# Kernel tuning notes

Hardware: AMD Instinct MI355X
Metric: run time of the kernel (lower is better)

The kernel has to match this reference:

```python
import jax, jax.numpy as jnp
import numpy as np

DIM = 768
HEADS = 12
HEAD_DIM = DIM // HEADS  # 64, must equal 2*ROPE_DIM
HIDDEN = int(DIM * 4 * 2 / 3)  # 2048
EPS = 1e-6


def _ln(x, w, b, eps=EPS):
    mu = jnp.mean(x, -1, keepdims=True)
    var = jnp.mean((x - mu) ** 2, -1, keepdims=True)
    return (x - mu) * jax.lax.rsqrt(var + eps) * w + b


def _rotate_half(x):
    xr = x.reshape(x.shape[:-1] + (-1, 2))
    return jnp.stack((-xr[..., 1], xr[..., 0]), -1).reshape(x.shape)


def _rope_tables(H, W):
    # Matches get_rope: dim=32 per axis, pt_seq_len=16, theta=10000
    dim, pt, theta = 32, 16.0, 10000.0
    freqs = 1.0 / theta ** (np.arange(0, dim, 2, dtype=np.float32) / dim)  # [16]
    fH = np.repeat((np.arange(H, dtype=np.float32) / H * pt)[:, None] * freqs[None, :], 2, axis=-1)  # [H,32]
    fW = np.repeat((np.arange(W, dtype=np.float32) / W * pt)[:, None] * freqs[None, :], 2, axis=-1)  # [W,32]
    f = np.concatenate([np.broadcast_to(fH[:, None, :], (H, W, dim)),
                        np.broadcast_to(fW[None, :, :], (H, W, dim))], -1)  # [H,W,64]
    f = f.reshape(H * W, 2 * dim)
    return jnp.asarray(np.cos(f)), jnp.asarray(np.sin(f))


def block_forward(x, ln1_w, ln1_b, q_w, q_b, k_w, v_w, v_b, proj_w, proj_b,
                  ln2_w, ln2_b, w1_w, w1_b, w2_w, w2_b, ffn_w, ffn_b, w3_w, w3_b, ws):
    B, H, W, C = x.shape
    shortcut = x
    h = _ln(x, ln1_w, ln1_b)
    # window partition with padding
    pad_h = (-H) % ws
    pad_w = (-W) % ws
    h = jnp.pad(h, ((0, 0), (0, pad_h), (0, pad_w), (0, 0)))
    Hp, Wp = H + pad_h, W + pad_w
    h = h.reshape(B, Hp // ws, ws, Wp // ws, ws, C).transpose(0, 1, 3, 2, 4, 5).reshape(-1, ws, ws, C)
    Bw = h.shape[0]
    N = ws * ws
    t = h.reshape(Bw, N, C)
    q = t @ q_w + q_b  # k has no bias
    k = t @ k_w
    v = t @ v_w + v_b
    q = q.reshape(Bw, N, HEADS, HEAD_DIM).transpose(0, 2, 1, 3)  # [Bw,h,N,d]
    k = k.reshape(Bw, N, HEADS, HEAD_DIM).transpose(0, 2, 1, 3)
    v = v.reshape(Bw, N, HEADS, HEAD_DIM).transpose(0, 2, 1, 3)
    cos, sin = _rope_tables(ws, ws)  # [N, 64]
    q = q * cos + _rotate_half(q) * sin
    k = k * cos + _rotate_half(k) * sin
    scale = HEAD_DIM ** (-0.5)
    attn = jax.nn.softmax(jnp.einsum('bhnd,bhmd->bhnm', q * scale, k), axis=-1)
    o = jnp.einsum('bhnm,bhmd->bhnd', attn, v).transpose(0, 2, 1, 3).reshape(Bw, N, -1)
    o = o @ proj_w + proj_b
    o = o.reshape(Bw, ws, ws, C)
    # window unpartition
    o = o.reshape(B, Hp // ws, Wp // ws, ws, ws, C).transpose(0, 1, 3, 2, 4, 5).reshape(B, Hp, Wp, C)
    o = o[:, :H, :W, :]
    x = shortcut + o
    # SwiGLU MLP with sub-LN
    h = _ln(x, ln2_w, ln2_b)
    hid = jax.nn.silu(h @ w1_w + w1_b) * (h @ w2_w + w2_b)
    hid = _ln(hid, ffn_w, ffn_b)
    return x + hid @ w3_w + w3_b


def setup_inputs() -> dict:
    key = jax.random.key(0)
    ks = jax.random.split(key, 9)
    s = 0.02
    d = {
        'x': jax.random.normal(ks[0], (8, 64, 64, DIM), jnp.float32),
        'ln1_w': jnp.ones((DIM,), jnp.float32),
        'ln1_b': jnp.zeros((DIM,), jnp.float32),
        'q_w': jax.random.normal(ks[1], (DIM, DIM), jnp.float32) * s,
        'q_b': jnp.zeros((DIM,), jnp.float32),
        'k_w': jax.random.normal(ks[2], (DIM, DIM), jnp.float32) * s,
        'v_w': jax.random.normal(ks[3], (DIM, DIM), jnp.float32) * s,
        'v_b': jnp.zeros((DIM,), jnp.float32),
        'proj_w': jax.random.normal(ks[4], (DIM, DIM), jnp.float32) * s,
        'proj_b': jnp.zeros((DIM,), jnp.float32),
        'ln2_w': jnp.ones((DIM,), jnp.float32),
        'ln2_b': jnp.zeros((DIM,), jnp.float32),
        'w1_w': jax.random.normal(ks[5], (DIM, HIDDEN), jnp.float32) * s,
        'w1_b': jnp.zeros((HIDDEN,), jnp.float32),
        'w2_w': jax.random.normal(ks[6], (DIM, HIDDEN), jnp.float32) * s,
        'w2_b': jnp.zeros((HIDDEN,), jnp.float32),
        'ffn_w': jnp.ones((HIDDEN,), jnp.float32),
        'ffn_b': jnp.zeros((HIDDEN,), jnp.float32),
        'w3_w': jax.random.normal(ks[7], (HIDDEN, DIM), jnp.float32) * s,
        'w3_b': jnp.zeros((DIM,), jnp.float32),
        'window_size': 14,
    }
    return d


def reference(x, ln1_w, ln1_b, q_w, q_b, k_w, v_w, v_b, proj_w, proj_b,
              ln2_w, ln2_b, w1_w, w1_b, w2_w, w2_b, ffn_w, ffn_b, w3_w, w3_b, window_size):
    return block_forward(x, ln1_w, ln1_b, q_w, q_b, k_w, v_w, v_b, proj_w, proj_b,
                         ln2_w, ln2_b, w1_w, w1_b, w2_w, w2_b, ffn_w, ffn_b, w3_w, w3_b,
                         int(window_size))
```

## Files before the change

kernel.cpp:

```cpp
#include <hip/hip_runtime.h>
#include <hip/hip_bf16.h>
#include <stdint.h>

typedef unsigned short u16;
typedef unsigned int u32;
typedef __attribute__((ext_vector_type(4))) float f32x4;
typedef __attribute__((ext_vector_type(8))) short s16x8;
typedef __attribute__((ext_vector_type(4))) u32 u32x4;

#define DEV __device__ __forceinline__
#define AS1 __attribute__((address_space(1)))
#define AS3 __attribute__((address_space(3)))

constexpr int T2 = 8 * 64 * 64;
constexpr int C = 768;
constexpr int HID = 2048;
constexpr int CHUNK = 8192;
constexpr int QKVS = 2304;

DEV float blo(u32 u) { return __uint_as_float(u << 16); }
DEV float bhi(u32 u) { return __uint_as_float(u & 0xffff0000u); }
DEV float b2f(u16 u) { return __uint_as_float((u32)u << 16); }
DEV u16 f2bf(float f) {
  u32 x = __float_as_uint(f);
  u32 r = x + 0x7fffu + ((x >> 16) & 1u);
  return (u16)(r >> 16);
}
DEV u32 pack2(float a, float b) { return (u32)f2bf(a) | ((u32)f2bf(b) << 16); }
DEV u32 cvtpk(float lo, float hi) {
  u32 r;
  asm("v_cvt_pk_bf16_f32 %0, %1, %2" : "=v"(r) : "v"(lo), "v"(hi));
  return r;
}

template <int NW>
DEV void reduce2(float& s, float& q) {
#pragma unroll
  for (int o = 32; o > 0; o >>= 1) {
    s += __shfl_down(s, o);
    q += __shfl_down(q, o);
  }
  __shared__ float ps[2 * NW];
  int wave = threadIdx.x >> 6, lane = threadIdx.x & 63;
  if (lane == 0) { ps[wave] = s; ps[NW + wave] = q; }
  __syncthreads();
  s = 0.f; q = 0.f;
#pragma unroll
  for (int i = 0; i < NW; ++i) { s += ps[i]; q += ps[NW + i]; }
}

__global__ __launch_bounds__(256) void transpose_cvt_tiled_k(
    const float* __restrict__ src, u16* __restrict__ dst, int K, int N, int rs, int ro) {
  __shared__ float t[32][33];
  int k0 = blockIdx.x * 32, n0 = blockIdx.y * 32;
  int tx = threadIdx.x, ty = threadIdx.y;
#pragma unroll
  for (int j = 0; j < 4; ++j)
    t[ty + j * 8][tx] = src[(size_t)(k0 + ty + j * 8) * N + n0 + tx];
  __syncthreads();
#pragma unroll
  for (int j = 0; j < 4; ++j) {
    int n = n0 + ty + j * 8;
    dst[((size_t)n * rs + ro) * K + k0 + tx] = f2bf(t[tx][ty + j * 8]);
  }
}

__global__ void build_biases_k(const float* __restrict__ qb, const float* __restrict__ vbb,
                               const float* __restrict__ w1b, const float* __restrict__ w2b,
                               float* __restrict__ qkvb, float* __restrict__ w12b) {
  int i = blockIdx.x * 256 + threadIdx.x;
  if (i < 2304)
    qkvb[i] = i < 768 ? qb[i] : (i < 1536 ? 0.f : vbb[i - 1536]);
  int j = i - 2304;
  if (j >= 0 && j < 4096) w12b[j] = (j & 1) ? w2b[j >> 1] : w1b[j >> 1];
}

__global__ void rope_tables_k(float* __restrict__ ct, float* __restrict__ st) {
  int i = blockIdx.x * 256 + threadIdx.x;
  if (i >= 196 * 32) return;
  int n = i >> 5, jp = i & 31;
  int d = jp << 1;
  int r = n / 14, c = n - r * 14;
  float pos, fj;
  if (d < 32) { pos = (float)r * (16.f / 14.f); fj = (float)(d >> 1); }
  else        { pos = (float)c * (16.f / 14.f); fj = (float)((d - 32) >> 1); }
  float fr = __expf(fj * (-2.f / 32.f) * logf(10000.f));
  float ang = pos * fr;
  float cv = cosf(ang), sv = sinf(ang);
  ct[n * 64 + d] = cv; ct[n * 64 + d + 1] = cv;
  st[n * 64 + d] = sv; st[n * 64 + d + 1] = sv;
}

__global__ __launch_bounds__(256) void ln_k(const float* __restrict__ in,
    const float* __restrict__ w, const float* __restrict__ bb, u16* __restrict__ out) {
  size_t row = blockIdx.x;
  int tid = threadIdx.x;
  const float* xr = in + row * C;
  float v0 = xr[tid], v1 = xr[tid + 256], v2 = xr[tid + 512];
  float s = v0 + v1 + v2, q = v0 * v0 + v1 * v1 + v2 * v2;
  reduce2<4>(s, q);
  float mu = s * (1.f / 768.f), var = q * (1.f / 768.f) - mu * mu;
  float rs = rsqrtf(var + 1e-6f);
  u16* orow = out + row * C;
  orow[tid]       = f2bf((v0 - mu) * rs * w[tid]       + bb[tid]);
  orow[tid + 256] = f2bf((v1 - mu) * rs * w[tid + 256] + bb[tid + 256]);
  orow[tid + 512] = f2bf((v2 - mu) * rs * w[tid + 512] + bb[tid + 512]);
}

__global__ __launch_bounds__(384) void ln_bf16_k(const u16* __restrict__ in,
    const float* __restrict__ w, const float* __restrict__ bb, u16* __restrict__ out) {
  size_t row = blockIdx.x;
  int t = threadIdx.x;
  u32 u = ((const u32*)(in + row * C))[t];
  float v0 = blo(u), v1 = bhi(u);
  float s = v0 + v1, q = v0 * v0 + v1 * v1;
  reduce2<6>(s, q);
  float mu = s * (1.f / 768.f), var = q * (1.f / 768.f) - mu * mu;
  float rs = rsqrtf(var + 1e-6f);
  float o0 = (v0 - mu) * rs * w[2 * t] + bb[2 * t];
  float o1 = (v1 - mu) * rs * w[2 * t + 1] + bb[2 * t + 1];
  ((u32*)(out + row * C))[t] = cvtpk(o0, o1);
}

DEV float rope1(float v, float p, int r, int d, bool odd, bool isq,
                const float* __restrict__ ct, const float* __restrict__ st) {
  int rem = r & 4095;
  int n = ((rem >> 6) % 14) * 14 + ((rem & 63) % 14);
  float c = ct[n * 64 + d], s = st[n * 64 + d];
  float o = odd ? (v * c + p * s) : (v * c - p * s);
  return isq ? o * 0.125f : o;
}

template <int EPI>
__global__ __launch_bounds__(256) void gemm_k(
    const u16* __restrict__ A, const u16* __restrict__ Bt,
    const float* __restrict__ bias, void* __restrict__ Cout,
    const void* __restrict__ resid, int M, int Nn, int K, int lda,
    const float* __restrict__ ct, const float* __restrict__ st) {
  __shared__ u16 LDS[128 * 128];
  u16* As = LDS;
  u16* Bs = LDS + 8192;
  const int tid = threadIdx.x;
  const int wave = tid >> 6, lane = tid & 63;
  const int wm = wave >> 1, wn = wave & 1;
  const int gx = gridDim.x;
  const int id = blockIdx.y * gx + blockIdx.x;
  const int xcd = id & 7;
  const int j0 = id >> 3;
  const int W = gx >> 3;
  const int per_sub = gridDim.y << 3;
  const int sub = j0 / per_sub;
  const int jj = j0 - sub * per_sub;
  const int tm = xcd * W + (sub << 3) + (jj & 7);
  const int tn = jj >> 3;
  const int l16 = lane & 15, lq = lane >> 4;

  f32x4 acc[4][4];
#pragma unroll
  for (int a = 0; a < 4; ++a)
#pragma unroll
    for (int b = 0; b < 4; ++b)
#pragma unroll
      for (int e = 0; e < 4; ++e) acc[a][b][e] = 0.f;

  const int nk = K >> 6;
  for (int kt = 0; kt < nk; ++kt) {
    const int k0 = kt << 6;
#pragma unroll
    for (int i = 0; i < 4; ++i) {
      int row = (((wave << 2) + i) << 3) + (lane >> 3);
      int cl = (lane & 7) ^ (row & 7);
      const u16* sa = A + (size_t)(tm * 128 + row) * lda + k0 + cl * 8;
      __builtin_amdgcn_global_load_lds((const AS1 u32*)sa,
          (AS3 u32*)(As + (((wave << 2) + i) << 9)), 16, 0, 0);
      const u16* sb = Bt + (size_t)(tn * 128 + row) * K + k0 + cl * 8;
      __builtin_amdgcn_global_load_lds((const AS1 u32*)sb,
          (AS3 u32*)(Bs + (((wave << 2) + i) << 9)), 16, 0, 0);
    }
    asm volatile("s_waitcnt vmcnt(0)" ::: "memory");
    __syncthreads();
#pragma unroll
    for (int ks = 0; ks < 2; ++ks) {
      s16x8 af[4], bfr[4];
#pragma unroll
      for (int mf = 0; mf < 4; ++mf) {
        int row = (wm << 6) + (mf << 4) + l16;
        int sc = ((ks << 2) + lq) ^ (row & 7);
        af[mf] = *(const s16x8*)(As + row * 64 + sc * 8);
      }
#pragma unroll
      for (int nf = 0; nf < 4; ++nf) {
        int row = (wn << 6) + (nf << 4) + l16;
        int sc = ((ks << 2) + lq) ^ (row & 7);
        bfr[nf] = *(const s16x8*)(Bs + row * 64 + sc * 8);
      }
      __builtin_amdgcn_s_setprio(1);
#pragma unroll
      for (int mf = 0; mf < 4; ++mf)
#pragma unroll
        for (int nf = 0; nf < 4; ++nf)
          acc[mf][nf] =
              __builtin_amdgcn_mfma_f32_16x16x32_bf16(af[mf], bfr[nf], acc[mf][nf], 0, 0, 0);
      __builtin_amdgcn_s_setprio(0);
    }
    __syncthreads();
  }

  if constexpr (EPI == 2) {
#pragma unroll
    for (int nf = 0; nf < 4; ++nf) {
      int col = (tn << 7) + (wn << 6) + (nf << 4) + l16;
      float bs = bias[col];
      const u16* rp = (const u16*)resid;
#pragma unroll
      for (int mf = 0; mf < 4; ++mf) {
        int rbase = (tm << 7) + (wm << 6) + (mf << 4) + (lq << 2);
#pragma unroll
        for (int j = 0; j < 4; ++j) {
          size_t idx = (size_t)(rbase + j) * Nn + col;
          ((float*)Cout)[idx] = b2f(rp[idx]) + acc[mf][nf][j] + bs;
        }
      }
    }
  } else {
#pragma unroll
    for (int nf = 0; nf < 4; ++nf) {
      int lcol = (wn << 6) + (nf << 4) + l16;
      int col = (tn << 7) + lcol;
      float bs = bias[col];
#pragma unroll
      for (int mf = 0; mf < 4; ++mf) {
        int rloc = (wm << 6) + (mf << 4) + (lq << 2);
        float v[4];
#pragma unroll
        for (int j = 0; j < 4; ++j) v[j] = acc[mf][nf][j] + bs;
        if constexpr (EPI == 1) {
          const float* rp = (const float*)resid;
#pragma unroll
          for (int j = 0; j < 4; ++j)
            v[j] += rp[(size_t)(tm * 128 + rloc + j) * Nn + col];
        }
        if constexpr (EPI == 3) {
          float pv[4];
#pragma unroll
          for (int j = 0; j < 4; ++j) pv[j] = __shfl_xor(v[j], 1);
          if (col < 1536) {
            bool odd = (l16 & 1) != 0, isq = col < 768;
            int d = col & 63;
#pragma unroll
            for (int j = 0; j < 4; ++j)
              v[j] = rope1(v[j], pv[j], tm * 128 + rloc + j, d, odd, isq, ct, st);
          }
        }
#pragma unroll
        for (int j = 0; j < 4; ++j) {
          int row = rloc + j;
          int byte = row * 256 + ((lcol * 2) ^ ((row & 7) << 4));
          *(u16*)((char*)LDS + byte) = f2bf(v[j]);
        }
      }
    }
    __syncthreads();
    u16* Cb = (u16*)Cout + (size_t)(tm * 128) * Nn + (tn << 7);
    int chunk = tid & 15;
#pragma unroll
    for (int it = 0; it < 8; ++it) {
      int row = (tid >> 4) + it * 16;
      int byte = row * 256 + ((chunk * 16) ^ ((row & 7) << 4));
      u32x4 val = *(const u32x4*)((const char*)LDS + byte);
      *(u32x4*)(Cb + (size_t)row * Nn + chunk * 8) = val;
    }
  }
}

__global__ __launch_bounds__(256) void attn_mfma_k(u16* __restrict__ qkv,
    const float* __restrict__ vb) {
  __shared__ u16 Vt[64 * 224];
  __shared__ u16 Pl[4 * 16 * 40];
  __shared__ int rowTab[208];
  int wid = blockIdx.x / 12, h = blockIdx.x - wid * 12;
  int bi = wid / 25, wr = wid - bi * 25;
  int hi = wr / 5, wj = wr - hi * 5;
  int rh = (hi == 4) ? 8 : 14, rw = (wj == 4) ? 8 : 14;
  int nv = rh * rw;
  int nk16 = (nv + 15) >> 4;
  int kvfull = nk16 >> 1;
  int nsteps = kvfull + (nk16 & 1);
  int vcols = ((nk16 + 1) >> 1) << 5;
  int tid = threadIdx.x;
  int rowbase = (bi * 64 + hi * 14) * 64 + wj * 14;

  if (tid < 208) {
    int mk = tid < nv ? tid : nv - 1;
    int nr = mk / rw, nc = mk - nr * rw;
    rowTab[tid] = rowbase + nr * 64 + nc;
  }
  __syncthreads();
  for (int idx = tid; idx < vcols * 32; idx += 256) {
    int key = idx >> 5, dp = idx & 31;
    int d = dp << 1;
    u32 val;
    if (key < nv) {
      size_t off = (size_t)rowTab[key] * QKVS + 1536 + (h << 6) + d;
      val = *(const u32*)(qkv + off);
    } else {
      val = pack2(vb[(h << 6) + d], vb[(h << 6) + d + 1]);
    }
    int b0 = (d * 448 + key * 2) ^ ((d & 7) << 4);
    int b1 = ((d + 1) * 448 + key * 2) ^ (((d + 1) & 7) << 4);
    Vt[b0 >> 1] = (u16)(val & 0xffffu);
    Vt[b1 >> 1] = (u16)(val >> 16);
  }
  __syncthreads();

  int wave = tid >> 6, lane = tid & 63;
  int l16 = lane & 15, lq = lane >> 4;
  u16* Pw = Pl + wave * 640;
  const u16* kbase = qkv + 768 + (h << 6);
  float vbr[4];
#pragma unroll
  for (int dt = 0; dt < 4; ++dt) vbr[dt] = vb[(h << 6) + dt * 16 + l16];

  int mtiles = (nv + 15) >> 4;
  for (int mt = wave; mt < mtiles; mt += 4) {
    s16x8 a[2];
    {
      int qi = mt * 16 + l16;
      const u16* qp = qkv + (size_t)rowTab[qi] * QKVS + (h << 6);
      a[0] = *(const s16x8*)(qp + lq * 8);
      a[1] = *(const s16x8*)(qp + 32 + lq * 8);
    }
    f32x4 O[4];
#pragma unroll
    for (int dt = 0; dt < 4; ++dt)
#pragma unroll
      for (int j = 0; j < 4; ++j) O[dt][j] = 0.f;
    float lrow[4] = {0.f, 0.f, 0.f, 0.f};

    for (int kv = 0; kv < nsteps; ++kv) {
      const bool full = kv < kvfull;
      const int keyb = kv << 5;
      f32x4 s0 = {0.f, 0.f, 0.f, 0.f}, s1 = {0.f, 0.f, 0.f, 0.f};
      int key0 = keyb + l16, key1 = key0 + 16;
      const u16* kr0 = kbase + (size_t)rowTab[key0] * QKVS;
      const u16* kr1 = full ? (kbase + (size_t)rowTab[key1] * QKVS) : kbase;
      __builtin_amdgcn_s_setprio(1);
#pragma unroll
      for (int s = 0; s < 2; ++s) {
        s16x8 b0 = *(const s16x8*)(kr0 + s * 32 + lq * 8);
        s0 = __builtin_amdgcn_mfma_f32_16x16x32_bf16(a[s], b0, s0, 0, 0, 0);
        if (full) {
          s16x8 b1 = *(const s16x8*)(kr1 + s * 32 + lq * 8);
          s1 = __builtin_amdgcn_mfma_f32_16x16x32_bf16(a[s], b1, s1, 0, 0, 0);
        }
      }
      __builtin_amdgcn_s_setprio(0);
#pragma unroll
      for (int j = 0; j < 4; ++j) {
        float p0 = key0 < nv ? __expf(s0[j]) : (key0 < 196 ? 1.f : 0.f);
        float p1 = full ? (key1 < nv ? __expf(s1[j]) : (key1 < 196 ? 1.f : 0.f)) : 0.f;
        float rs = p0 + p1;
        rs += __shfl_xor(rs, 1);
        rs += __shfl_xor(rs, 2);
        rs += __shfl_xor(rs, 4);
        rs += __shfl_xor(rs, 8);
        lrow[j] += rs;
        u32 pk = cvtpk(p0, p1);
        Pw[(lq * 4 + j) * 40 + l16] = (u16)pk;
        Pw[(lq * 4 + j) * 40 + l16 + 16] = (u16)(pk >> 16);
      }
      s16x8 pa = *(const s16x8*)(Pw + l16 * 40 + lq * 8);
      __builtin_amdgcn_s_setprio(1);
#pragma unroll
      for (int dt = 0; dt < 4; ++dt) {
        int d = dt * 16 + l16;
        int vbyte = (d * 448 + keyb * 2 + lq * 16) ^ ((d & 7) << 4);
        s16x8 bv = *(const s16x8*)(Vt + (vbyte >> 1));
        O[dt] = __builtin_amdgcn_mfma_f32_16x16x32_bf16(pa, bv, O[dt], 0, 0, 0);
      }
      __builtin_amdgcn_s_setprio(0);
    }
    int Prem = 196 - (nk16 << 4);
    if (Prem > 0) {
#pragma unroll
      for (int j = 0; j < 4; ++j) {
        lrow[j] += (float)Prem;
#pragma unroll
        for (int dt = 0; dt < 4; ++dt) O[dt][j] += (float)Prem * vbr[dt];
      }
    }
#pragma unroll
    for (int j = 0; j < 4; ++j) {
      int qi = mt * 16 + lq * 4 + j;
      if (qi < nv) {
        float inv = 1.f / lrow[j];
        u16* op = qkv + (size_t)rowTab[qi] * QKVS + (h << 6);
#pragma unroll
        for (int dt = 0; dt < 4; ++dt) op[dt * 16 + l16] = f2bf(O[dt][j] * inv);
      }
    }
  }
}

__global__ __launch_bounds__(256) void swiglu_ln_k(u16* __restrict__ h12,
    const float* __restrict__ w, const float* __restrict__ bb) {
  size_t row = blockIdx.x;
  int tid = threadIdx.x;
  const u32x4 ua = *(const u32x4*)(h12 + row * 4096 + tid * 16);
  const u32x4 ub = *(const u32x4*)(h12 + row * 4096 + tid * 16 + 8);
  u32 pp[8] = {ua.x, ua.y, ua.z, ua.w, ub.x, ub.y, ub.z, ub.w};
  float g[8];
  float s = 0.f, qq = 0.f;
#pragma unroll
  for (int j = 0; j < 8; ++j) {
    float a = blo(pp[j]), b = bhi(pp[j]);
    float sl = a / (1.f + __expf(-a));
    g[j] = sl * b;
    s += g[j];
    qq += g[j] * g[j];
  }
  reduce2<4>(s, qq);
  float mu = s * (1.f / 2048.f);
  float var = qq * (1.f / 2048.f) - mu * mu;
  float rs = rsqrtf(var + 1e-6f);
  const float* wp = w + tid * 8;
  const float* bp = bb + tid * 8;
  u32 o4[4];
#pragma unroll
  for (int j = 0; j < 4; ++j) {
    float o0 = (g[2 * j] - mu) * rs * wp[2 * j] + bp[2 * j];
    float o1 = (g[2 * j + 1] - mu) * rs * wp[2 * j + 1] + bp[2 * j + 1];
    o4[j] = cvtpk(o0, o1);
  }
  *(u32x4*)(h12 + row * 4096 + tid * 8) = (u32x4){o4[0], o4[1], o4[2], o4[3]};
}

extern "C" void kernel_launch(void* const* d_in, const int* in_sizes, int n_in,
                              void* d_out, int out_size, void* d_ws, size_t ws_size,
                              hipStream_t stream) {
  const float* x    = (const float*)d_in[0];
  const float* ln1w = (const float*)d_in[1];
  const float* ln1b = (const float*)d_in[2];
  const float* qw   = (const float*)d_in[3];
  const float* qb   = (const float*)d_in[4];
  const float* kw   = (const float*)d_in[5];
  const float* vw   = (const float*)d_in[6];
  const float* vb   = (const float*)d_in[7];
  const float* pw   = (const float*)d_in[8];
  const float* pb   = (const float*)d_in[9];
  const float* ln2w = (const float*)d_in[10];
  const float* ln2b = (const float*)d_in[11];
  const float* w1   = (const float*)d_in[12];
  const float* w1b  = (const float*)d_in[13];
  const float* w2   = (const float*)d_in[14];
  const float* w2b  = (const float*)d_in[15];
  const float* ffw  = (const float*)d_in[16];
  const float* ffb  = (const float*)d_in[17];
  const float* w3   = (const float*)d_in[18];
  const float* w3b  = (const float*)d_in[19];

  char* ws = (char*)d_ws;
  size_t off = 0;
  auto alloc = [&](size_t bytes) -> char* {
    char* p = ws + off;
    off += (bytes + 255) & ~(size_t)255;
    return p;
  };
  u16* qkvwt = (u16*)alloc((size_t)QKVS * 768 * 2);
  u16* pwt   = (u16*)alloc((size_t)768 * 768 * 2);
  u16* w12t  = (u16*)alloc((size_t)4096 * 768 * 2);
  u16* w3t   = (u16*)alloc((size_t)768 * 2048 * 2);
  float* qkvb = (float*)alloc((size_t)QKVS * 4);
  float* w12b = (float*)alloc((size_t)4096 * 4);
  float* ct = (float*)alloc((size_t)196 * 64 * 4);
  float* st = (float*)alloc((size_t)196 * 64 * 4);
  u16* xw  = (u16*)alloc((size_t)T2 * C * 2);
  u16* qkv = (u16*)alloc((size_t)T2 * QKVS * 2);
  u16* x2b  = xw;
  u16* h2   = qkv;
  u16* h12c = qkv + (size_t)T2 * C;
  float* outp = (float*)d_out;

  dim3 tb(32, 8);
  transpose_cvt_tiled_k<<<dim3(24, 24), tb, 0, stream>>>(qw, qkvwt, 768, 768, 1, 0);
  transpose_cvt_tiled_k<<<dim3(24, 24), tb, 0, stream>>>(kw, qkvwt + (size_t)768 * 768, 768, 768, 1, 0);
  transpose_cvt_tiled_k<<<dim3(24, 24), tb, 0, stream>>>(vw, qkvwt + (size_t)1536 * 768, 768, 768, 1, 0);
  transpose_cvt_tiled_k<<<dim3(24, 24), tb, 0, stream>>>(pw, pwt, 768, 768, 1, 0);
  transpose_cvt_tiled_k<<<dim3(24, 64), tb, 0, stream>>>(w1, w12t, 768, 2048, 2, 0);
  transpose_cvt_tiled_k<<<dim3(24, 64), tb, 0, stream>>>(w2, w12t, 768, 2048, 2, 1);
  transpose_cvt_tiled_k<<<dim3(64, 24), tb, 0, stream>>>(w3, w3t, 2048, 768, 1, 0);
  build_biases_k<<<25, 256, 0, stream>>>(qb, vb, w1b, w2b, qkvb, w12b);
  rope_tables_k<<<(196 * 32 + 255) / 256, 256, 0, stream>>>(ct, st);

  ln_k<<<T2, 256, 0, stream>>>(x, ln1w, ln1b, xw);
  gemm_k<3><<<dim3(T2 / 128, QKVS / 128), 256, 0, stream>>>(
      xw, qkvwt, qkvb, qkv, nullptr, T2, QKVS, 768, 768, ct, st);
  attn_mfma_k<<<200 * 12, 256, 0, stream>>>(qkv, vb);
  gemm_k<1><<<dim3(T2 / 128, 6), 256, 0, stream>>>(
      qkv, pwt, pb, x2b, x, T2, 768, 768, QKVS, nullptr, nullptr);

  ln_bf16_k<<<T2, 384, 0, stream>>>(x2b, ln2w, ln2b, h2);
  for (int cidx = 0; cidx < T2 / CHUNK; ++cidx) {
    const u16* hrow = h2 + (size_t)cidx * CHUNK * C;
    gemm_k<0><<<dim3(CHUNK / 128, 32), 256, 0, stream>>>(
        hrow, w12t, w12b, h12c, nullptr, CHUNK, 4096, 768, 768, nullptr, nullptr);
    swiglu_ln_k<<<CHUNK, 256, 0, stream>>>(h12c, ffw, ffb);
    gemm_k<2><<<dim3(CHUNK / 128, 6), 256, 0, stream>>>(
        h12c, w3t, w3b, outp + (size_t)cidx * CHUNK * C,
        x2b + (size_t)cidx * CHUNK * C, CHUNK, 768, 2048, 4096, nullptr, nullptr);
  }
}
```

Baseline: 1.059 ms.

## Add 256x256 double-buffered GEMM with async LDS loads and fused RoPE epilogue

Adds a new 512-thread GEMM kernel with 256x256 output tiles, double-buffered LDS staging through global_load_lds, and a prefetch of the next K tile during compute. It is used for the QKV, projection and W1/W2 GEMMs. RoPE moves to the coalesced store phase using a packed cos/sin float2 table, replacing per-element table loads and shuffles. The W3 GEMM stays on the old 128-tile kernel, now specialised to its residual epilogue. The 128KB LDS footprint and larger accumulator arrays limit occupancy, and the bigger tiles mean fewer blocks for the smaller GEMMs.

```diff
diff --git a/kernel.cpp b/kernel.cpp
--- a/kernel.cpp
+++ b/kernel.cpp
@@ -75,20 +75,17 @@
   if (j >= 0 && j < 4096) w12b[j] = (j & 1) ? w2b[j >> 1] : w1b[j >> 1];
 }
 
-__global__ void rope_tables_k(float* __restrict__ ct, float* __restrict__ st) {
+__global__ void rope_tables_k(float2* __restrict__ csp) {
   int i = blockIdx.x * 256 + threadIdx.x;
   if (i >= 196 * 32) return;
-  int n = i >> 5, jp = i & 31;
-  int d = jp << 1;
+  int n = i >> 5, dp = i & 31;
   int r = n / 14, c = n - r * 14;
   float pos, fj;
-  if (d < 32) { pos = (float)r * (16.f / 14.f); fj = (float)(d >> 1); }
-  else        { pos = (float)c * (16.f / 14.f); fj = (float)((d - 32) >> 1); }
+  if (dp < 16) { pos = (float)r * (16.f / 14.f); fj = (float)dp; }
+  else         { pos = (float)c * (16.f / 14.f); fj = (float)(dp - 16); }
   float fr = __expf(fj * (-2.f / 32.f) * logf(10000.f));
   float ang = pos * fr;
-  float cv = cosf(ang), sv = sinf(ang);
-  ct[n * 64 + d] = cv; ct[n * 64 + d + 1] = cv;
-  st[n * 64 + d] = sv; st[n * 64 + d + 1] = sv;
+  csp[i] = make_float2(cosf(ang), sinf(ang));
 }
 
 __global__ __launch_bounds__(256) void ln_k(const float* __restrict__ in,
@@ -122,24 +119,155 @@
   ((u32*)(out + row * C))[t] = cvtpk(o0, o1);
 }
 
-DEV float rope1(float v, float p, int r, int d, bool odd, bool isq,
-                const float* __restrict__ ct, const float* __restrict__ st) {
-  int rem = r & 4095;
-  int n = ((rem >> 6) % 14) * 14 + ((rem & 63) % 14);
-  float c = ct[n * 64 + d], s = st[n * 64 + d];
-  float o = odd ? (v * c + p * s) : (v * c - p * s);
-  return isq ? o * 0.125f : o;
-}
-
 template <int EPI>
-__global__ __launch_bounds__(256) void gemm_k(
+__global__ __launch_bounds__(512, 2) void gemm256_k(
     const u16* __restrict__ A, const u16* __restrict__ Bt,
     const float* __restrict__ bias, void* __restrict__ Cout,
     const void* __restrict__ resid, int M, int Nn, int K, int lda,
-    const float* __restrict__ ct, const float* __restrict__ st) {
-  __shared__ u16 LDS[128 * 128];
-  u16* As = LDS;
-  u16* Bs = LDS + 8192;
+    const float2* __restrict__ csp) {
+  __shared__ u16 LDS[65536];
+  const int tid = threadIdx.x;
+  const int wave = tid >> 6, lane = tid & 63;
+  const int wm = wave >> 2, wn = wave & 3;
+  const int l16 = lane & 15, lq = lane >> 4;
+  const int gx = gridDim.x;
+  const int id = blockIdx.y * gx + blockIdx.x;
+  const int xcd = id & 7;
+  const int j0 = id >> 3;
+  const int W = gx >> 3;
+  const int SW = W < 8 ? W : 8;
+  const int per_sub = gridDim.y * SW;
+  const int sub = j0 / per_sub;
+  const int jj = j0 - sub * per_sub;
+  const int tm = xcd * W + sub * SW + (jj & (SW - 1));
+  const int tn = jj / SW;
+
+  f32x4 acc[8][4];
+#pragma unroll
+  for (int a = 0; a < 8; ++a)
+#pragma unroll
+    for (int b = 0; b < 4; ++b)
+#pragma unroll
+      for (int e = 0; e < 4; ++e) acc[a][b][e] = 0.f;
+
+  const int nk = K >> 6;
+  auto STAGE = [&](int kt, int buf) {
+    const int k0 = kt << 6;
+    u16* Ad = LDS + buf * 32768;
+    u16* Bd = Ad + 16384;
+#pragma unroll
+    for (int i = 0; i < 4; ++i) {
+      int blk = (wave << 2) + i;
+      int row = (blk << 3) + (lane >> 3);
+      int cl = (lane & 7) ^ (row & 7);
+      const u16* sa = A + (size_t)(tm * 256 + row) * lda + k0 + cl * 8;
+      __builtin_amdgcn_global_load_lds((const AS1 u32*)sa, (AS3 u32*)(Ad + (blk << 9)),
+                                       16, 0, 0);
+      const u16* sb = Bt + (size_t)(tn * 256 + row) * K + k0 + cl * 8;
+      __builtin_amdgcn_global_load_lds((const AS1 u32*)sb, (AS3 u32*)(Bd + (blk << 9)),
+                                       16, 0, 0);
+    }
+  };
+
+  STAGE(0, 0);
+  asm volatile("s_waitcnt vmcnt(0)" ::: "memory");
+  __syncthreads();
+  for (int t = 0; t < nk; ++t) {
+    const int cur = t & 1;
+    if (t + 1 < nk) STAGE(t + 1, cur ^ 1);
+    const u16* As = LDS + cur * 32768;
+    const u16* Bs = As + 16384;
+#pragma unroll
+    for (int ks = 0; ks < 2; ++ks) {
+      s16x8 bfr[4];
+#pragma unroll
+      for (int nf = 0; nf < 4; ++nf) {
+        int row = (wn << 6) + (nf << 4) + l16;
+        int sc = ((ks << 2) + lq) ^ (row & 7);
+        bfr[nf] = *(const s16x8*)(Bs + row * 64 + sc * 8);
+      }
+      __builtin_amdgcn_s_setprio(1);
+#pragma unroll
+      for (int mf = 0; mf < 8; ++mf) {
+        int row = (wm << 7) + (mf << 4) + l16;
+        int sc = ((ks << 2) + lq) ^ (row & 7);
+        s16x8 af = *(const s16x8*)(As + row * 64 + sc * 8);
+#pragma unroll
+        for (int nf = 0; nf < 4; ++nf)
+          acc[mf][nf] =
+              __builtin_amdgcn_mfma_f32_16x16x32_bf16(af, bfr[nf], acc[mf][nf], 0, 0, 0);
+      }
+      __builtin_amdgcn_s_setprio(0);
+    }
+    asm volatile("s_waitcnt vmcnt(0)" ::: "memory");
+    __syncthreads();
+  }
+
+#pragma unroll
+  for (int nf = 0; nf < 4; ++nf) {
+    int lcol = (wn << 6) + (nf << 4) + l16;
+    int col = (tn << 8) + lcol;
+    float bs = bias[col];
+#pragma unroll
+    for (int mf = 0; mf < 8; ++mf) {
+      int rloc = (wm << 7) + (mf << 4) + (lq << 2);
+      float v[4];
+#pragma unroll
+      for (int j = 0; j < 4; ++j) v[j] = acc[mf][nf][j] + bs;
+      if constexpr (EPI == 1) {
+        const float* rp = (const float*)resid;
+#pragma unroll
+        for (int j = 0; j < 4; ++j)
+          v[j] += rp[(size_t)(tm * 256 + rloc + j) * Nn + col];
+      }
+#pragma unroll
+      for (int j = 0; j < 4; ++j) {
+        int row = rloc + j;
+        int byte = row * 512 + ((lcol * 2) ^ ((row & 7) << 4));
+        *(u16*)((char*)LDS + byte) = f2bf(v[j]);
+      }
+    }
+  }
+  __syncthreads();
+  u16* Cb = (u16*)Cout + (size_t)(tm * 256) * Nn + (tn << 8);
+  const int chunk = tid & 31;
+  const int cbase = (tn << 8) + chunk * 8;
+  const bool inqk = cbase < 1536, isq = cbase < 768;
+  const int dp0 = (cbase & 63) >> 1;
+#pragma unroll
+  for (int it = 0; it < 16; ++it) {
+    int row = (tid >> 5) + it * 16;
+    int byte = row * 512 + ((chunk * 16) ^ ((row & 7) << 4));
+    u32x4 val = *(const u32x4*)((const char*)LDS + byte);
+    if constexpr (EPI == 3) {
+      if (inqk) {
+        int tok = tm * 256 + row;
+        int rem = tok & 4095;
+        int n = ((rem >> 6) % 14) * 14 + ((rem & 63) % 14);
+        const float2* cp = csp + n * 32 + dp0;
+        u32 wv[4] = {val.x, val.y, val.z, val.w};
+#pragma unroll
+        for (int p = 0; p < 4; ++p) {
+          float2 cs = cp[p];
+          float e = blo(wv[p]), o = bhi(wv[p]);
+          float re = e * cs.x - o * cs.y;
+          float ro = o * cs.x + e * cs.y;
+          if (isq) { re *= 0.125f; ro *= 0.125f; }
+          wv[p] = cvtpk(re, ro);
+        }
+        val = (u32x4){wv[0], wv[1], wv[2], wv[3]};
+      }
+    }
+    *(u32x4*)(Cb + (size_t)row * Nn + chunk * 8) = val;
+  }
+}
+
+__global__ __launch_bounds__(256) void gemm_k(
+    const u16* __restrict__ A, const u16* __restrict__ Bt,
+    const float* __restrict__ bias, float* __restrict__ Cout,
+    const u16* __restrict__ resid, int M, int Nn, int K, int lda) {
+  __shared__ u16 As[128 * 64];
+  __shared__ u16 Bs[128 * 64];
   const int tid = threadIdx.x;
   const int wave = tid >> 6, lane = tid & 63;
   const int wm = wave >> 1, wn = wave & 1;
@@ -148,11 +276,12 @@
   const int xcd = id & 7;
   const int j0 = id >> 3;
   const int W = gx >> 3;
-  const int per_sub = gridDim.y << 3;
+  const int SW = W < 8 ? W : 8;
+  const int per_sub = gridDim.y * SW;
   const int sub = j0 / per_sub;
   const int jj = j0 - sub * per_sub;
-  const int tm = xcd * W + (sub << 3) + (jj & 7);
-  const int tn = jj >> 3;
+  const int tm = xcd * W + sub * SW + (jj & (SW - 1));
+  const int tn = jj / SW;
   const int l16 = lane & 15, lq = lane >> 4;
 
   f32x4 acc[4][4];
@@ -205,70 +334,18 @@
     }
     __syncthreads();
   }
-
-  if constexpr (EPI == 2) {
-#pragma unroll
-    for (int nf = 0; nf < 4; ++nf) {
-      int col = (tn << 7) + (wn << 6) + (nf << 4) + l16;
-      float bs = bias[col];
-      const u16* rp = (const u16*)resid;
-#pragma unroll
-      for (int mf = 0; mf < 4; ++mf) {
-        int rbase = (tm << 7) + (wm << 6) + (mf << 4) + (lq << 2);
-#pragma unroll
-        for (int j = 0; j < 4; ++j) {
-          size_t idx = (size_t)(rbase + j) * Nn + col;
-          ((float*)Cout)[idx] = b2f(rp[idx]) + acc[mf][nf][j] + bs;
-        }
-      }
-    }
-  } else {
-#pragma unroll
-    for (int nf = 0; nf < 4; ++nf) {
-      int lcol = (wn << 6) + (nf << 4) + l16;
-      int col = (tn << 7) + lcol;
-      float bs = bias[col];
-#pragma unroll
-      for (int mf = 0; mf < 4; ++mf) {
-        int rloc = (wm << 6) + (mf << 4) + (lq << 2);
-        float v[4];
-#pragma unroll
-        for (int j = 0; j < 4; ++j) v[j] = acc[mf][nf][j] + bs;
-        if constexpr (EPI == 1) {
-          const float* rp = (const float*)resid;
-#pragma unroll
-          for (int j = 0; j < 4; ++j)
-            v[j] += rp[(size_t)(tm * 128 + rloc + j) * Nn + col];
-        }
-        if constexpr (EPI == 3) {
-          float pv[4];
-#pragma unroll
-          for (int j = 0; j < 4; ++j) pv[j] = __shfl_xor(v[j], 1);
-          if (col < 1536) {
-            bool odd = (l16 & 1) != 0, isq = col < 768;
-            int d = col & 63;
-#pragma unroll
-            for (int j = 0; j < 4; ++j)
-              v[j] = rope1(v[j], pv[j], tm * 128 + rloc + j, d, odd, isq, ct, st);
-          }
-        }
-#pragma unroll
-        for (int j = 0; j < 4; ++j) {
-          int row = rloc + j;
-          int byte = row * 256 + ((lcol * 2) ^ ((row & 7) << 4));
-          *(u16*)((char*)LDS + byte) = f2bf(v[j]);
-        }
-      }
-    }
-    __syncthreads();
-    u16* Cb = (u16*)Cout + (size_t)(tm * 128) * Nn + (tn << 7);
-    int chunk = tid & 15;
-#pragma unroll
-    for (int it = 0; it < 8; ++it) {
-      int row = (tid >> 4) + it * 16;
-      int byte = row * 256 + ((chunk * 16) ^ ((row & 7) << 4));
-      u32x4 val = *(const u32x4*)((const char*)LDS + byte);
-      *(u32x4*)(Cb + (size_t)row * Nn + chunk * 8) = val;
+#pragma unroll
+  for (int nf = 0; nf < 4; ++nf) {
+    int col = (tn << 7) + (wn << 6) + (nf << 4) + l16;
+    float bs = bias[col];
+#pragma unroll
+    for (int mf = 0; mf < 4; ++mf) {
+      int rbase = (tm << 7) + (wm << 6) + (mf << 4) + (lq << 2);
+#pragma unroll
+      for (int j = 0; j < 4; ++j) {
+        size_t idx = (size_t)(rbase + j) * Nn + col;
+        Cout[idx] = b2f(resid[idx]) + acc[mf][nf][j] + bs;
+      }
     }
   }
 }
@@ -472,8 +549,7 @@
   u16* w3t   = (u16*)alloc((size_t)768 * 2048 * 2);
   float* qkvb = (float*)alloc((size_t)QKVS * 4);
   float* w12b = (float*)alloc((size_t)4096 * 4);
-  float* ct = (float*)alloc((size_t)196 * 64 * 4);
-  float* st = (float*)alloc((size_t)196 * 64 * 4);
+  float2* csp = (float2*)alloc((size_t)196 * 32 * 8);
   u16* xw  = (u16*)alloc((size_t)T2 * C * 2);
   u16* qkv = (u16*)alloc((size_t)T2 * QKVS * 2);
   u16* x2b  = xw;
@@ -490,23 +566,23 @@
   transpose_cvt_tiled_k<<<dim3(24, 64), tb, 0, stream>>>(w2, w12t, 768, 2048, 2, 1);
   transpose_cvt_tiled_k<<<dim3(64, 24), tb, 0, stream>>>(w3, w3t, 2048, 768, 1, 0);
   build_biases_k<<<25, 256, 0, stream>>>(qb, vb, w1b, w2b, qkvb, w12b);
-  rope_tables_k<<<(196 * 32 + 255) / 256, 256, 0, stream>>>(ct, st);
+  rope_tables_k<<<25, 256, 0, stream>>>(csp);
 
   ln_k<<<T2, 256, 0, stream>>>(x, ln1w, ln1b, xw);
-  gemm_k<3><<<dim3(T2 / 128, QKVS / 128), 256, 0, stream>>>(
-      xw, qkvwt, qkvb, qkv, nullptr, T2, QKVS, 768, 768, ct, st);
+  gemm256_k<3><<<dim3(T2 / 256, QKVS / 256), 512, 0, stream>>>(
+      xw, qkvwt, qkvb, qkv, nullptr, T2, QKVS, 768, 768, csp);
   attn_mfma_k<<<200 * 12, 256, 0, stream>>>(qkv, vb);
-  gemm_k<1><<<dim3(T2 / 128, 6), 256, 0, stream>>>(
-      qkv, pwt, pb, x2b, x, T2, 768, 768, QKVS, nullptr, nullptr);
+  gemm256_k<1><<<dim3(T2 / 256, 3), 512, 0, stream>>>(
+      qkv, pwt, pb, x2b, x, T2, 768, 768, QKVS, nullptr);
 
   ln_bf16_k<<<T2, 384, 0, stream>>>(x2b, ln2w, ln2b, h2);
   for (int cidx = 0; cidx < T2 / CHUNK; ++cidx) {
     const u16* hrow = h2 + (size_t)cidx * CHUNK * C;
-    gemm_k<0><<<dim3(CHUNK / 128, 32), 256, 0, stream>>>(
-        hrow, w12t, w12b, h12c, nullptr, CHUNK, 4096, 768, 768, nullptr, nullptr);
+    gemm256_k<0><<<dim3(CHUNK / 256, 16), 512, 0, stream>>>(
+        hrow, w12t, w12b, h12c, nullptr, CHUNK, 4096, 768, 768, nullptr);
     swiglu_ln_k<<<CHUNK, 256, 0, stream>>>(h12c, ffw, ffb);
-    gemm_k<2><<<dim3(CHUNK / 128, 6), 256, 0, stream>>>(
+    gemm_k<<<dim3(CHUNK / 128, 6), 256, 0, stream>>>(
         h12c, w3t, w3b, outp + (size_t)cidx * CHUNK * C,
-        x2b + (size_t)cidx * CHUNK * C, CHUNK, 768, 2048, 4096, nullptr, nullptr);
-  }
-}
+        x2b + (size_t)cidx * CHUNK * C, CHUNK, 768, 2048, 4096);
+  }
+}
```

Result: faster. 932.9 us (-11.9%).
